# Kernel tuning notes

Hardware: AMD Instinct MI355X
Metric: run time of the kernel (lower is better)

Reference implementation:

```python
import jax, jax.numpy as jnp
import numpy as np

DIM = 1024
N_HEADS = 16
HEAD_DIM = DIM // N_HEADS
MAX_SEQ_LEN = 2048
B, T = 2, 2048


def build_rope_cache(max_seq_len, head_dim):
    half_dim = head_dim // 2
    freq_seq = jnp.arange(half_dim, dtype=jnp.float32)
    inv_freq = 1.0 / 10000.0 ** (freq_seq / half_dim)
    t = jnp.arange(max_seq_len, dtype=jnp.float32)
    freqs = jnp.outer(t, inv_freq)                      # [S, half]
    emb = jnp.concatenate((freqs, freqs), axis=-1)      # [S, head_dim]
    cos = jnp.cos(emb)[None, :, None, :]                # [1, S, 1, head_dim]
    sin = jnp.sin(emb)[None, :, None, :]
    return cos, sin


def apply_rope(x, cos, sin):
    # x: [B, T, H, Dh]; cos/sin: [1, T, 1, Dh]
    x_even = x[..., ::2]
    x_odd = x[..., 1::2]
    cos_even = cos[..., ::2]
    sin_even = sin[..., ::2]
    x_even_rot = x_even * cos_even - x_odd * sin_even
    x_odd_rot = x_even * sin_even + x_odd * cos_even
    x_rot = jnp.stack([x_even_rot, x_odd_rot], axis=-1)  # [B,T,H,Dh/2,2]
    return x_rot.reshape(x.shape)


def setup_inputs() -> dict:
    key = jax.random.key(0)
    k1, k2, k3, k4, k5 = jax.random.split(key, 5)
    s = 0.02
    return {
        "x": jax.random.normal(k1, (B, T, DIM), dtype=jnp.float32),
        "attention_mask": jnp.ones((B, T), dtype=bool),
        "qkv_w": jax.random.normal(k2, (3 * DIM, DIM), dtype=jnp.float32) * s,
        "qkv_b": jax.random.normal(k3, (3 * DIM,), dtype=jnp.float32) * s,
        "out_w": jax.random.normal(k4, (DIM, DIM), dtype=jnp.float32) * s,
        "out_b": jax.random.normal(k5, (DIM,), dtype=jnp.float32) * s,
    }


def reference(x, attention_mask, qkv_w, qkv_b, out_w, out_b):
    Bx, Tx, _ = x.shape
    H, Dh = N_HEADS, HEAD_DIM
    scale = Dh ** (-0.5)

    qkv = x @ qkv_w.T + qkv_b                            # [B,T,3*dim]
    qkv = qkv.reshape(Bx, Tx, 3, H, Dh)
    q, k, v = qkv[:, :, 0], qkv[:, :, 1], qkv[:, :, 2]   # [B,T,H,Dh]

    cos, sin = build_rope_cache(MAX_SEQ_LEN, Dh)
    cos_all = cos[:, :Tx]
    sin_all = sin[:, :Tx]
    k = apply_rope(k, cos_all, sin_all)
    q = apply_rope(q, cos_all, sin_all)  # past_len = 0

    scores = jnp.einsum("bthd,bshd->bhts", q, k) * scale  # [B,H,T,S]

    causal = jnp.arange(Tx)[None, :] <= jnp.arange(Tx)[:, None]  # [T,S]
    scores = jnp.where(causal[None, None, :, :], scores, -jnp.inf)
    pad = attention_mask[:, None, None, :]                        # [B,1,1,S]
    scores = jnp.where(pad, scores, -jnp.inf)

    probs = jax.nn.softmax(scores, axis=-1)
    out = jnp.einsum("bhts,bshd->bthd", probs, v)        # [B,T,H,Dh]
    out = out.reshape(Bx, Tx, H * Dh)
    out = out @ out_w.T + out_b
    return out
```

## Files before the change

kernel.cpp:

```cpp
#include <hip/hip_runtime.h>
#include <stdint.h>

#define B_    2
#define T_    2048
#define DIM_  1024
#define NH_   16
#define DH_   64
#define MTOK  (B_*T_)

typedef __attribute__((ext_vector_type(8))) short bf16x8;
typedef __attribute__((ext_vector_type(4))) float f32x4;
typedef __attribute__((ext_vector_type(4))) short short4v;

__device__ __forceinline__ short f2bf(float f){
  union { float f; uint32_t u; } v; v.f = f;
  uint32_t u = v.u;
  return (short)((u + 0x7fffu + ((u>>16)&1u)) >> 16);
}
__device__ __forceinline__ float fexp2(float x){
  float r; asm("v_exp_f32 %0, %1" : "=v"(r) : "v"(x)); return r;
}

#define GLDS(g, l) __builtin_amdgcn_global_load_lds( \
    (const __attribute__((address_space(1))) void*)(g), \
    (__attribute__((address_space(3))) void*)(l), 16, 0, 0)

__global__ void convert_all(const float* __restrict__ x, const float* __restrict__ wq,
                            const float* __restrict__ wo,
                            short* __restrict__ xb, short* __restrict__ wqb,
                            short* __restrict__ wob, float* __restrict__ tbl){
  const int NX = MTOK*DIM_/4;
  const int NW = 3*DIM_*DIM_/4;
  const int NO = DIM_*DIM_/4;
  const int total = NX + NW + NO;
  const int gtid = blockIdx.x*blockDim.x + threadIdx.x;
  if (gtid < T_*32){
    int t = gtid >> 5, j = gtid & 31;
    float f = powf(10000.f, -(float)((2*j) & 31) / 32.f);
    float ang = (float)t * f;
    tbl[gtid*2]   = cosf(ang);
    tbl[gtid*2+1] = sinf(ang);
  }
  for (int i = gtid; i < total; i += gridDim.x*blockDim.x){
    const float* src; short* dst; int j;
    if (i < NX){ src = x;  dst = xb;  j = i; }
    else if (i < NX+NW){ src = wq; dst = wqb; j = i-NX; }
    else { src = wo; dst = wob; j = i-NX-NW; }
    float4 v = ((const float4*)src)[j];
    short4v o;
    o.x = f2bf(v.x); o.y = f2bf(v.y); o.z = f2bf(v.z); o.w = f2bf(v.w);
    ((short4v*)dst)[j] = o;
  }
}

__global__ __launch_bounds__(256,2)
void gemm192_qkv(const short* __restrict__ A, const short* __restrict__ Bw,
                 const float* __restrict__ bias,
                 short* __restrict__ qb, short* __restrict__ kb, short* __restrict__ vb,
                 const float* __restrict__ rtbl)
{
  extern __shared__ char smem[];
  const int K = 1024, nt = 16;
  const int tid = threadIdx.x;
  const int wave = tid >> 6, lane = tid & 63;
  const int lid = blockIdx.x + blockIdx.y * 16;
  const int bx = ((lid & 7) << 1) | ((lid >> 3) & 1);
  const int by = lid >> 4;
  const int bm = by << 7;
  const int bn = bx * 192;
  const int wm = (wave >> 1) << 6;
  const int wn = (wave & 1) * 96;
  const int r16 = lane & 15, g4 = lane >> 4;
  const int slr = lane >> 3, slc = (lane & 7) << 4;

  f32x4 acc[4][6] = {};

  auto stage = [&](int t, int slot){
    char* As = smem + slot * 40960;
    char* Bs = As + 16384;
    const int k0 = t << 6;
    #pragma unroll
    for (int sg = 0; sg < 4; ++sg){
      int row = (wave << 5) + (sg << 3) + slr;
      GLDS((const char*)A + ((size_t)(bm + row)*K + k0)*2 + (slc ^ ((row&7)<<4)),
           As + ((wave << 5) + (sg << 3))*128);
    }
    #pragma unroll
    for (int sg = 0; sg < 6; ++sg){
      int row = wave*48 + (sg << 3) + slr;
      GLDS((const char*)Bw + ((size_t)(bn + row)*K + k0)*2 + (slc ^ ((row&7)<<4)),
           Bs + (wave*48 + (sg << 3))*128);
    }
  };

  stage(0, 0);
  for (int t = 0; t < nt; ++t){
    if (t + 1 < nt) stage(t + 1, (t + 1) & 1);
    if (t + 1 < nt) asm volatile("s_waitcnt vmcnt(10)" ::: "memory");
    else            asm volatile("s_waitcnt vmcnt(0)"  ::: "memory");
    __builtin_amdgcn_s_barrier();
    asm volatile("" ::: "memory");
    char* As = smem + (t & 1) * 40960;
    char* Bs = As + 16384;
    #pragma unroll
    for (int ks = 0; ks < 2; ++ks){
      bf16x8 af[4], bfr[6];
      int bo = (ks << 6) + (g4 << 4);
      #pragma unroll
      for (int mf = 0; mf < 4; ++mf){
        int row = wm + (mf << 4) + r16;
        af[mf] = *(const bf16x8*)(As + row*128 + (bo ^ ((row&7)<<4)));
      }
      #pragma unroll
      for (int nf = 0; nf < 6; ++nf){
        int row = wn + (nf << 4) + r16;
        bfr[nf] = *(const bf16x8*)(Bs + row*128 + (bo ^ ((row&7)<<4)));
      }
      __builtin_amdgcn_s_setprio(1);
      #pragma unroll
      for (int mf = 0; mf < 4; ++mf)
        #pragma unroll
        for (int nf = 0; nf < 6; ++nf)
          acc[mf][nf] = __builtin_amdgcn_mfma_f32_16x16x32_bf16(af[mf], bfr[nf], acc[mf][nf], 0, 0, 0);
      __builtin_amdgcn_s_setprio(0);
    }
    asm volatile("" ::: "memory");
    __builtin_amdgcn_s_barrier();
  }

  #pragma unroll
  for (int nf = 0; nf < 6; ++nf){
    int gn = bn + wn + (nf << 4) + r16;
    int s = gn >> 10;
    int d = gn & 63, h = (gn >> 6) & 15;
    float bv = bias[gn];
    if (s < 2){
      short* dst = s ? kb : qb;
      const float scq = s ? 1.0f : 0.18033688f;
      int u = d >> 1;
      float sgn = (d & 1) ? 1.f : -1.f;
      #pragma unroll
      for (int mf = 0; mf < 4; ++mf){
        #pragma unroll
        for (int j = 0; j < 4; ++j){
          int gm = bm + wm + (mf << 4) + (g4 << 2) + j;
          int b = gm >> 11, t = gm & (T_-1);
          float val = acc[mf][nf][j] + bv;
          float prt = __shfl_xor(val, 1);
          float2 cssn = ((const float2*)rtbl)[(t << 5) + u];
          float out = (val*cssn.x + prt*sgn*cssn.y) * scq;
          dst[(((size_t)(b*NH_+h))*T_ + t)*DH_ + d] = f2bf(out);
        }
      }
    } else {
      #pragma unroll
      for (int mf = 0; mf < 4; ++mf){
        int gm0 = bm + wm + (mf << 4) + (g4 << 2);
        int b = gm0 >> 11, t0 = gm0 & (T_-1);
        short* vrow = vb + ((size_t)((b*NH_+h)*DH_ + d))*T_ + (t0 & ~63);
        int lo = t0 & 15, hi = (t0 & 63) >> 4;
        #pragma unroll
        for (int j = 0; j < 4; ++j)
          vrow[((lo + j) << 2) + hi] = f2bf(acc[mf][nf][j] + bv);
      }
    }
  }
}

__global__ __launch_bounds__(256,2)
void gemm_out(const short* __restrict__ A, const short* __restrict__ Bw,
              const float* __restrict__ bias, float* __restrict__ outf)
{
  extern __shared__ char smem[];
  const int K = 1024, nt = 16;
  const int tid = threadIdx.x;
  const int wave = tid >> 6, lane = tid & 63;
  const int lid = blockIdx.x + blockIdx.y * 16;
  const int bx = ((lid & 7) << 1) | ((lid >> 3) & 1);
  const int by = lid >> 4;
  const int bm = by << 7;
  const int bn = bx << 6;
  const int wm = (wave >> 1) << 6;
  const int wn = (wave & 1) << 5;
  const int r16 = lane & 15, g4 = lane >> 4;
  const int slr = lane >> 3, slc = (lane & 7) << 4;

  f32x4 acc[4][2] = {};

  auto stage = [&](int t, int slot){
    char* As = smem + slot * 24576;
    char* Bs = As + 16384;
    const int k0 = t << 6;
    #pragma unroll
    for (int sg = 0; sg < 4; ++sg){
      int row = (wave << 5) + (sg << 3) + slr;
      GLDS((const char*)A + ((size_t)(bm + row)*K + k0)*2 + (slc ^ ((row&7)<<4)),
           As + ((wave << 5) + (sg << 3))*128);
    }
    #pragma unroll
    for (int sg = 0; sg < 2; ++sg){
      int row = (wave << 4) + (sg << 3) + slr;
      GLDS((const char*)Bw + ((size_t)(bn + row)*K + k0)*2 + (slc ^ ((row&7)<<4)),
           Bs + ((wave << 4) + (sg << 3))*128);
    }
  };

  stage(0, 0);
  for (int t = 0; t < nt; ++t){
    if (t + 1 < nt) stage(t + 1, (t + 1) & 1);
    if (t + 1 < nt) asm volatile("s_waitcnt vmcnt(6)" ::: "memory");
    else            asm volatile("s_waitcnt vmcnt(0)" ::: "memory");
    __builtin_amdgcn_s_barrier();
    asm volatile("" ::: "memory");
    char* As = smem + (t & 1) * 24576;
    char* Bs = As + 16384;
    #pragma unroll
    for (int ks = 0; ks < 2; ++ks){
      bf16x8 af[4], bfr[2];
      int bo = (ks << 6) + (g4 << 4);
      #pragma unroll
      for (int mf = 0; mf < 4; ++mf){
        int row = wm + (mf << 4) + r16;
        af[mf] = *(const bf16x8*)(As + row*128 + (bo ^ ((row&7)<<4)));
      }
      #pragma unroll
      for (int nf = 0; nf < 2; ++nf){
        int row = wn + (nf << 4) + r16;
        bfr[nf] = *(const bf16x8*)(Bs + row*128 + (bo ^ ((row&7)<<4)));
      }
      __builtin_amdgcn_s_setprio(1);
      #pragma unroll
      for (int mf = 0; mf < 4; ++mf)
        #pragma unroll
        for (int nf = 0; nf < 2; ++nf)
          acc[mf][nf] = __builtin_amdgcn_mfma_f32_16x16x32_bf16(af[mf], bfr[nf], acc[mf][nf], 0, 0, 0);
      __builtin_amdgcn_s_setprio(0);
    }
    asm volatile("" ::: "memory");
    __builtin_amdgcn_s_barrier();
  }

  #pragma unroll
  for (int nf = 0; nf < 2; ++nf){
    int gn = bn + wn + (nf << 4) + r16;
    float bv = bias[gn];
    #pragma unroll
    for (int mf = 0; mf < 4; ++mf)
      #pragma unroll
      for (int j = 0; j < 4; ++j){
        int gm = bm + wm + (mf << 4) + (g4 << 2) + j;
        outf[(size_t)gm*DIM_ + gn] = acc[mf][nf][j] + bv;
      }
  }
}

__global__ __launch_bounds__(256,2)
void attn_fwd(const short* __restrict__ q, const short* __restrict__ k,
              const short* __restrict__ vt, short* __restrict__ o)
{
  __shared__ char smem[40960];
  const int lid = blockIdx.x + (blockIdx.y << 4);
  const int swzid = (lid & 7) * 64 + (lid >> 3);
  const int p = swzid & 15, bh = swzid >> 4;
  const int qtA = 31 - p, qtB = p;
  const int tid = threadIdx.x, wave = tid >> 6, lane = tid & 63;
  char* Ps = smem + 32768 + wave*2048;
  const int r16 = lane & 15, g4 = lane >> 4;
  const int slr = lane >> 3, slc = (lane & 7) << 4;

  bf16x8 qfA[2], qfB[2];
  {
    size_t qrA = ((size_t)bh*T_ + (qtA<<6) + (wave<<4) + r16) * DH_;
    qfA[0] = *(const bf16x8*)(q + qrA + (g4<<3));
    qfA[1] = *(const bf16x8*)(q + qrA + 32 + (g4<<3));
    size_t qrB = ((size_t)bh*T_ + (qtB<<6) + (wave<<4) + r16) * DH_;
    qfB[0] = *(const bf16x8*)(q + qrB + (g4<<3));
    qfB[1] = *(const bf16x8*)(q + qrB + 32 + (g4<<3));
  }
  f32x4 oaccA[4] = {}, oaccB[4] = {};
  float rsA[4] = {0.f,0.f,0.f,0.f}, rsB[4] = {0.f,0.f,0.f,0.f};

  auto stage = [&](int c, int buf){
    char* Kb = smem + buf*8192;
    char* Vb = smem + 16384 + buf*8192;
    #pragma unroll
    for (int sg = 0; sg < 2; ++sg){
      int row = (wave<<4) + (sg<<3) + slr;
      const char* sk = (const char*)k  + (((size_t)bh*T_ + (c<<6) + row)*DH_)*2 + (slc ^ ((row&7)<<4));
      GLDS(sk, Kb + ((wave<<4)+(sg<<3))*128);
      const char* sv = (const char*)vt + (((size_t)bh*DH_ + row)*T_ + (c<<6))*2 + (slc ^ ((row&7)<<4));
      GLDS(sv, Vb + ((wave<<4)+(sg<<3))*128);
    }
  };

  stage(0, 0);
  asm volatile("s_waitcnt vmcnt(0)" ::: "memory");
  __syncthreads();

  for (int c = 0; c <= qtA; ++c){
    const int cur = c & 1;
    if (c < qtA) stage(c+1, cur^1);
    char* Kb = smem + cur*8192;
    char* Vb = smem + 16384 + cur*8192;

    #pragma unroll
    for (int tile = 0; tile < 2; ++tile){
      if (tile == 1 && c > qtB) break;
      const bf16x8* qf = tile ? qfB : qfA;
      f32x4* oacc = tile ? oaccB : oaccA;
      float* rs = tile ? rsB : rsA;
      const bool diag = (c == (tile ? qtB : qtA));

      f32x4 sc[4] = {};
      __builtin_amdgcn_s_setprio(1);
      #pragma unroll
      for (int ks = 0; ks < 2; ++ks){
        int bo = (ks<<6) + (g4<<4);
        #pragma unroll
        for (int nf = 0; nf < 4; ++nf){
          int row = (nf<<4) + r16;
          bf16x8 bk = *(const bf16x8*)(Kb + row*128 + (bo ^ ((row&7)<<4)));
          sc[nf] = __builtin_amdgcn_mfma_f32_16x16x32_bf16(qf[ks], bk, sc[nf], 0, 0, 0);
        }
      }
      __builtin_amdgcn_s_setprio(0);
      #pragma unroll
      for (int nf = 0; nf < 4; ++nf){
        #pragma unroll
        for (int j = 0; j < 4; ++j){
          float pv;
          if (diag){
            int colr = (nf<<4) + r16;
            int rowr = (wave<<4) + (g4<<2) + j;
            pv = (colr > rowr) ? 0.f : fexp2(sc[nf][j]);
          } else {
            pv = fexp2(sc[nf][j]);
          }
          sc[nf][j] = pv;
          rs[j] += pv;
        }
      }
      #pragma unroll
      for (int j = 0; j < 4; ++j){
        int prow = (g4<<2) + j;
        uint32_t lo, hi;
        asm("v_cvt_pk_bf16_f32 %0, %1, %2" : "=v"(lo) : "v"(sc[0][j]), "v"(sc[1][j]));
        asm("v_cvt_pk_bf16_f32 %0, %1, %2" : "=v"(hi) : "v"(sc[2][j]), "v"(sc[3][j]));
        uint2 pk; pk.x = lo; pk.y = hi;
        *(uint2*)(Ps + prow*128 + ((r16<<3) ^ ((prow&7)<<4))) = pk;
      }
      #pragma unroll
      for (int ks = 0; ks < 2; ++ks){
        int bo = (ks<<6) + (g4<<4);
        bf16x8 pa = *(const bf16x8*)(Ps + r16*128 + (bo ^ ((r16&7)<<4)));
        __builtin_amdgcn_s_setprio(1);
        #pragma unroll
        for (int nf = 0; nf < 4; ++nf){
          int row = (nf<<4) + r16;
          bf16x8 bv = *(const bf16x8*)(Vb + row*128 + (bo ^ ((row&7)<<4)));
          oacc[nf] = __builtin_amdgcn_mfma_f32_16x16x32_bf16(pa, bv, oacc[nf], 0, 0, 0);
        }
        __builtin_amdgcn_s_setprio(0);
      }
    }
    asm volatile("s_waitcnt vmcnt(0)" ::: "memory");
    __syncthreads();
  }

  const int b = bh >> 4, h = bh & 15;
  #pragma unroll
  for (int tile = 0; tile < 2; ++tile){
    const int qt = tile ? qtB : qtA;
    f32x4* oacc = tile ? oaccB : oaccA;
    float* rs = tile ? rsB : rsA;
    #pragma unroll
    for (int j = 0; j < 4; ++j){
      float s = rs[j];
      #pragma unroll
      for (int off = 1; off < 16; off <<= 1) s += __shfl_xor(s, off);
      float inv = 1.f / s;
      int t = (qt<<6) + (wave<<4) + (g4<<2) + j;
      #pragma unroll
      for (int nf = 0; nf < 4; ++nf){
        int d = (nf<<4) + r16;
        o[((size_t)(b*T_ + t))*DIM_ + h*DH_ + d] = f2bf(oacc[nf][j]*inv);
      }
    }
  }
}

extern "C" void kernel_launch(void* const* d_in, const int* in_sizes, int n_in,
                              void* d_out, int out_size, void* d_ws, size_t ws_size,
                              hipStream_t stream){
  const float* x     = (const float*)d_in[0];
  const float* qkv_w = (const float*)d_in[2];
  const float* qkv_b = (const float*)d_in[3];
  const float* out_w = (const float*)d_in[4];
  const float* out_b = (const float*)d_in[5];

  char* ws = (char*)d_ws;
  size_t off = 0;
  auto alloc = [&](size_t bytes){ void* p = ws + off; off += (bytes + 255) & ~(size_t)255; return p; };

  short* xb   = (short*)alloc((size_t)MTOK*DIM_*2);
  short* wqb  = (short*)alloc((size_t)3*DIM_*DIM_*2);
  short* wob  = (short*)alloc((size_t)DIM_*DIM_*2);
  short* qbuf = (short*)alloc((size_t)B_*NH_*T_*DH_*2);
  short* kbuf = (short*)alloc((size_t)B_*NH_*T_*DH_*2);
  short* vtr  = (short*)alloc((size_t)B_*NH_*DH_*T_*2);
  short* aout = (short*)alloc((size_t)MTOK*DIM_*2);
  float* tbl  = (float*)alloc((size_t)T_*32*2*4);

  convert_all<<<2048, 256, 0, stream>>>(x, qkv_w, out_w, xb, wqb, wob, tbl);
  gemm192_qkv<<<dim3(16,32), 256, 81920, stream>>>(xb, wqb, qkv_b,
                                                   qbuf, kbuf, vtr, tbl);
  attn_fwd<<<dim3(16,32), 256, 0, stream>>>(qbuf, kbuf, vtr, aout);
  gemm_out<<<dim3(16,32), 256, 49152, stream>>>(aout, wob, out_b, (float*)d_out);
}
```

Baseline: 91.91 us.

## Rewrite QKV GEMM as 256x256 tile with 8 waves and quadrant-interleaved staging

Replaces the 128x192 QKV projection tile with a 256x256 tile computed by 512 threads (8 waves), using 128 KB of double-buffered LDS. Each k-step is split into four quadrant MFMA phases, and each phase issues one half of the next tile's A or B global-to-LDS loads, so loads overlap compute with finer-grained waits and barriers. The larger tile improves operand reuse per LDS byte, but the grid shrinks to 192 blocks. That may underfill the 256 CUs, and 128 KB of LDS limits residency.

```diff
diff --git a/kernel.cpp b/kernel.cpp
--- a/kernel.cpp
+++ b/kernel.cpp
@@ -53,84 +53,118 @@
   }
 }
 
-__global__ __launch_bounds__(256,2)
-void gemm192_qkv(const short* __restrict__ A, const short* __restrict__ Bw,
-                 const float* __restrict__ bias,
-                 short* __restrict__ qb, short* __restrict__ kb, short* __restrict__ vb,
-                 const float* __restrict__ rtbl)
+__global__ __launch_bounds__(512,2)
+void gemm256p_qkv(const short* __restrict__ A, const short* __restrict__ Bw,
+                  const float* __restrict__ bias,
+                  short* __restrict__ qb, short* __restrict__ kb, short* __restrict__ vb,
+                  const float* __restrict__ rtbl)
 {
   extern __shared__ char smem[];
   const int K = 1024, nt = 16;
   const int tid = threadIdx.x;
   const int wave = tid >> 6, lane = tid & 63;
-  const int lid = blockIdx.x + blockIdx.y * 16;
-  const int bx = ((lid & 7) << 1) | ((lid >> 3) & 1);
-  const int by = lid >> 4;
-  const int bm = by << 7;
-  const int bn = bx * 192;
-  const int wm = (wave >> 1) << 6;
-  const int wn = (wave & 1) * 96;
+  const int lid = blockIdx.x + blockIdx.y * 12;
+  const int swz = (lid & 7) * 24 + (lid >> 3);
+  const int bx = swz % 12, by = swz / 12;
+  const int bm = by << 8, bn = bx << 8;
+  const int wm = (wave >> 2) << 7;
+  const int wn = (wave & 3) << 6;
   const int r16 = lane & 15, g4 = lane >> 4;
-  const int slr = lane >> 3, slc = (lane & 7) << 4;
-
-  f32x4 acc[4][6] = {};
-
-  auto stage = [&](int t, int slot){
-    char* As = smem + slot * 40960;
-    char* Bs = As + 16384;
+
+  f32x4 acc[8][4] = {};
+
+  auto stage_half = [&](int t, int buf, int sel){
+    const bool isB = (sel >= 2);
+    const int h = sel & 1;
+    char* base = smem + buf*65536 + (isB ? 32768 : 0);
+    const short* src = isB ? Bw : A;
+    const int gb = isB ? bn : bm;
     const int k0 = t << 6;
     #pragma unroll
-    for (int sg = 0; sg < 4; ++sg){
-      int row = (wave << 5) + (sg << 3) + slr;
-      GLDS((const char*)A + ((size_t)(bm + row)*K + k0)*2 + (slc ^ ((row&7)<<4)),
-           As + ((wave << 5) + (sg << 3))*128);
-    }
-    #pragma unroll
-    for (int sg = 0; sg < 6; ++sg){
-      int row = wave*48 + (sg << 3) + slr;
-      GLDS((const char*)Bw + ((size_t)(bn + row)*K + k0)*2 + (slc ^ ((row&7)<<4)),
-           Bs + (wave*48 + (sg << 3))*128);
-    }
-  };
-
-  stage(0, 0);
+    for (int round = 0; round < 2; ++round){
+      int row = h*128 + round*64 + wave*8 + (lane >> 3);
+      int off = ((lane & 7) << 4) ^ ((row & 7) << 4);
+      GLDS((const char*)src + ((size_t)(gb + row)*K + k0)*2 + off,
+           base + (h*128 + round*64 + wave*8)*128);
+    }
+  };
+
+  auto read_af = [&](const char* Abuf, int mh, bf16x8 (&af)[8]){
+    #pragma unroll
+    for (int mf = 0; mf < 4; ++mf)
+      #pragma unroll
+      for (int ks = 0; ks < 2; ++ks){
+        int row = wm + mh*64 + (mf<<4) + r16;
+        int bo = (ks<<6) + (g4<<4);
+        af[mf*2+ks] = *(const bf16x8*)(Abuf + row*128 + (bo ^ ((row&7)<<4)));
+      }
+  };
+  auto read_bf = [&](const char* Bbuf, int nh, bf16x8 (&bf)[4]){
+    #pragma unroll
+    for (int nf = 0; nf < 2; ++nf)
+      #pragma unroll
+      for (int ks = 0; ks < 2; ++ks){
+        int row = wn + nh*32 + (nf<<4) + r16;
+        int bo = (ks<<6) + (g4<<4);
+        bf[nf*2+ks] = *(const bf16x8*)(Bbuf + row*128 + (bo ^ ((row&7)<<4)));
+      }
+  };
+  auto mfma_quad = [&](int mh, int nh, bf16x8 (&af)[8], bf16x8 (&bf)[4]){
+    __builtin_amdgcn_s_setprio(1);
+    #pragma unroll
+    for (int mf = 0; mf < 4; ++mf)
+      #pragma unroll
+      for (int nf = 0; nf < 2; ++nf)
+        #pragma unroll
+        for (int ks = 0; ks < 2; ++ks)
+          acc[mh*4+mf][nh*2+nf] = __builtin_amdgcn_mfma_f32_16x16x32_bf16(
+              af[mf*2+ks], bf[nf*2+ks], acc[mh*4+mf][nh*2+nf], 0, 0, 0);
+    __builtin_amdgcn_s_setprio(0);
+  };
+
+  bf16x8 af[8], bfr0[4], bfr1[4];
+
+  stage_half(0, 0, 0); stage_half(0, 0, 2); stage_half(0, 0, 3); stage_half(0, 0, 1);
+
   for (int t = 0; t < nt; ++t){
-    if (t + 1 < nt) stage(t + 1, (t + 1) & 1);
-    if (t + 1 < nt) asm volatile("s_waitcnt vmcnt(10)" ::: "memory");
-    else            asm volatile("s_waitcnt vmcnt(0)"  ::: "memory");
-    __builtin_amdgcn_s_barrier();
-    asm volatile("" ::: "memory");
-    char* As = smem + (t & 1) * 40960;
-    char* Bs = As + 16384;
-    #pragma unroll
-    for (int ks = 0; ks < 2; ++ks){
-      bf16x8 af[4], bfr[6];
-      int bo = (ks << 6) + (g4 << 4);
-      #pragma unroll
-      for (int mf = 0; mf < 4; ++mf){
-        int row = wm + (mf << 4) + r16;
-        af[mf] = *(const bf16x8*)(As + row*128 + (bo ^ ((row&7)<<4)));
-      }
-      #pragma unroll
-      for (int nf = 0; nf < 6; ++nf){
-        int row = wn + (nf << 4) + r16;
-        bfr[nf] = *(const bf16x8*)(Bs + row*128 + (bo ^ ((row&7)<<4)));
-      }
-      __builtin_amdgcn_s_setprio(1);
-      #pragma unroll
-      for (int mf = 0; mf < 4; ++mf)
-        #pragma unroll
-        for (int nf = 0; nf < 6; ++nf)
-          acc[mf][nf] = __builtin_amdgcn_mfma_f32_16x16x32_bf16(af[mf], bfr[nf], acc[mf][nf], 0, 0, 0);
-      __builtin_amdgcn_s_setprio(0);
-    }
-    asm volatile("" ::: "memory");
-    __builtin_amdgcn_s_barrier();
+    const char* Abuf = smem + (t & 1)*65536;
+    const char* Bbuf = Abuf + 32768;
+    const int nb = (t + 1) & 1;
+    const bool st = (t + 1 < nt);
+
+    asm volatile("s_waitcnt vmcnt(4)" ::: "memory");
+    __builtin_amdgcn_s_barrier();
+    asm volatile("" ::: "memory");
+    if (st) stage_half(t+1, nb, 0);
+    read_af(Abuf, 0, af);
+    read_bf(Bbuf, 0, bfr0);
+    mfma_quad(0, 0, af, bfr0);
+
+    if (st) asm volatile("s_waitcnt vmcnt(4)" ::: "memory");
+    else    asm volatile("s_waitcnt vmcnt(2)" ::: "memory");
+    __builtin_amdgcn_s_barrier();
+    asm volatile("" ::: "memory");
+    if (st) stage_half(t+1, nb, 2);
+    read_bf(Bbuf, 1, bfr1);
+    mfma_quad(0, 1, af, bfr1);
+
+    if (st) asm volatile("s_waitcnt vmcnt(4)" ::: "memory");
+    else    asm volatile("s_waitcnt vmcnt(0)" ::: "memory");
+    __builtin_amdgcn_s_barrier();
+    asm volatile("" ::: "memory");
+    if (st) stage_half(t+1, nb, 3);
+    read_af(Abuf, 1, af);
+    mfma_quad(1, 1, af, bfr1);
+
+    __builtin_amdgcn_s_barrier();
+    asm volatile("" ::: "memory");
+    if (st) stage_half(t+1, nb, 1);
+    mfma_quad(1, 0, af, bfr0);
   }
 
   #pragma unroll
-  for (int nf = 0; nf < 6; ++nf){
-    int gn = bn + wn + (nf << 4) + r16;
+  for (int b2 = 0; b2 < 4; ++b2){
+    int gn = bn + wn + ((b2>>1)<<5) + ((b2&1)<<4) + r16;
     int s = gn >> 10;
     int d = gn & 63, h = (gn >> 6) & 15;
     float bv = bias[gn];
@@ -140,12 +174,13 @@
       int u = d >> 1;
       float sgn = (d & 1) ? 1.f : -1.f;
       #pragma unroll
-      for (int mf = 0; mf < 4; ++mf){
+      for (int a = 0; a < 8; ++a){
+        int rowbase = bm + wm + ((a>>2)<<6) + ((a&3)<<4);
         #pragma unroll
         for (int j = 0; j < 4; ++j){
-          int gm = bm + wm + (mf << 4) + (g4 << 2) + j;
+          int gm = rowbase + (g4<<2) + j;
           int b = gm >> 11, t = gm & (T_-1);
-          float val = acc[mf][nf][j] + bv;
+          float val = acc[a][b2][j] + bv;
           float prt = __shfl_xor(val, 1);
           float2 cssn = ((const float2*)rtbl)[(t << 5) + u];
           float out = (val*cssn.x + prt*sgn*cssn.y) * scq;
@@ -154,14 +189,15 @@
       }
     } else {
       #pragma unroll
-      for (int mf = 0; mf < 4; ++mf){
-        int gm0 = bm + wm + (mf << 4) + (g4 << 2);
+      for (int a = 0; a < 8; ++a){
+        int rowbase = bm + wm + ((a>>2)<<6) + ((a&3)<<4);
+        int gm0 = rowbase + (g4<<2);
         int b = gm0 >> 11, t0 = gm0 & (T_-1);
         short* vrow = vb + ((size_t)((b*NH_+h)*DH_ + d))*T_ + (t0 & ~63);
         int lo = t0 & 15, hi = (t0 & 63) >> 4;
         #pragma unroll
         for (int j = 0; j < 4; ++j)
-          vrow[((lo + j) << 2) + hi] = f2bf(acc[mf][nf][j] + bv);
+          vrow[((lo + j) << 2) + hi] = f2bf(acc[a][b2][j] + bv);
       }
     }
   }
@@ -412,8 +448,8 @@
   float* tbl  = (float*)alloc((size_t)T_*32*2*4);
 
   convert_all<<<2048, 256, 0, stream>>>(x, qkv_w, out_w, xb, wqb, wob, tbl);
-  gemm192_qkv<<<dim3(16,32), 256, 81920, stream>>>(xb, wqb, qkv_b,
-                                                   qbuf, kbuf, vtr, tbl);
+  gemm256p_qkv<<<dim3(12,16), 512, 131072, stream>>>(xb, wqb, qkv_b,
+                                                     qbuf, kbuf, vtr, tbl);
   attn_fwd<<<dim3(16,32), 256, 0, stream>>>(qbuf, kbuf, vtr, aout);
   gemm_out<<<dim3(16,32), 256, 49152, stream>>>(aout, wob, out_b, (float*)d_out);
 }
```

Measured after the change: 96.02 us. 4.5% more time.
